# Kernel tuning notes

Measured on AMD Instinct MI355X. Metric: run time of the kernel, lower is better.

## Reference

```python
import jax, jax.numpy as jnp
import numpy as np

TOP_K = 2
NUM_EXPERTS = 64
TEMPERATURE = 1.0

def setup_inputs() -> dict:
    key = jax.random.key(0)
    ks = jax.random.split(key, 4)
    B, L, D, DT, E = 4, 4096, 2048, 16, NUM_EXPERTS
    return {
        "x": jax.random.normal(ks[0], (B, L, D), dtype=jnp.float32),
        "z_task": jax.random.normal(ks[1], (B, DT), dtype=jnp.float32),
        "W_router": jax.random.normal(ks[2], (E, D + DT), dtype=jnp.float32) * 0.02,
        "W_task_proj": jax.random.normal(ks[3], (DT, DT), dtype=jnp.float32) * 0.25,
        "b_task_proj": jnp.zeros((DT,), dtype=jnp.float32),
        "expert_bias": jnp.zeros((E,), dtype=jnp.float32),
    }

def reference(x, z_task, W_router, W_task_proj, b_task_proj, expert_bias):
    B, L, D = x.shape
    E = W_router.shape[0]
    DT = z_task.shape[-1]
    # task_proj: Linear(d_task, d_task) + exact GELU
    tp = jax.nn.gelu(z_task @ W_task_proj.T + b_task_proj, approximate=False)  # [B, DT]
    # concat fusion: logits = [x ; task_proj] @ W_router^T, split to avoid materializing concat
    logits = (jnp.einsum('bld,ed->ble', x, W_router[:, :D])
              + jnp.einsum('bt,et->be', tp, W_router[:, D:])[:, None, :]
              + expert_bias)  # [B, L, E]
    probs = jax.nn.softmax(logits / TEMPERATURE, axis=-1)
    topw, topi = jax.lax.top_k(probs, TOP_K)  # [B, L, K]
    topw = topw / (topw.sum(axis=-1, keepdims=True) + 1e-8)
    # aux load-balance loss: E * sum_i f_i * P_i over flattened tokens
    mask = jax.nn.one_hot(topi, E, dtype=probs.dtype).sum(axis=-2) / TOP_K  # [B, L, E]
    f = mask.reshape(-1, E).mean(axis=0)
    P = probs.reshape(-1, E).mean(axis=0)
    aux_loss = E * (f * P).sum()
    return topw, topi, probs, aux_loss
```

## Files before the change

kernel.cpp:

```cpp
#include <hip/hip_runtime.h>
#include <math.h>


#define DDIM 2048
#define WROW 2064

typedef unsigned int u32;
typedef unsigned short u16;
typedef unsigned long long u64;
using short8 = __attribute__((ext_vector_type(8))) short;
using f32x4  = __attribute__((ext_vector_type(4))) float;

typedef const __attribute__((address_space(1))) u32* gp1;
typedef __attribute__((address_space(3))) u32* lp3;

#define BAR() do {                                                              \
        __builtin_amdgcn_s_barrier();                                           \
        asm volatile("" ::: "memory");                                          \
        __builtin_amdgcn_sched_barrier(0);                                      \
    } while (0)

__device__ __forceinline__ u16 bf16rne(float f) {
    u32 u = __float_as_uint(f);
    return (u16)((u + 0x7FFFu + ((u >> 16) & 1u)) >> 16);
}

__global__ void k0_wsplit(const float* __restrict__ Wr, u32* __restrict__ wh,
                          u32* __restrict__ wl) {
    const int g = blockIdx.x * 256 + threadIdx.x;
    const int e  = g >> 10;
    const int kp = g & 1023;
    const int k  = kp * 2;
    const int step = k >> 5, kb = (k >> 3) & 3, d = (k >> 1) & 3;
    const int grp = e >> 4, lane = kb * 16 + (e & 15);
    const float w0 = Wr[(size_t)e * WROW + k];
    const float w1 = Wr[(size_t)e * WROW + k + 1];
    const u16 h0 = bf16rne(w0);
    const u16 h1 = bf16rne(w1);
    const u16 l0 = bf16rne(w0 - __uint_as_float((u32)h0 << 16));
    const u16 l1 = bf16rne(w1 - __uint_as_float((u32)h1 << 16));
    const u32 oi = (u32)(((step * 4 + grp) * 64 + lane) * 4 + d);
    wh[oi] = ((u32)h1 << 16) | h0;
    wl[oi] = ((u32)l1 << 16) | l0;
}

__global__ void k1_task(const float* __restrict__ z, const float* __restrict__ Wp,
                        const float* __restrict__ bp, const float* __restrict__ Wr,
                        const float* __restrict__ eb, float* __restrict__ wsb) {
    __shared__ float tp[4][16];
    const int t = threadIdx.x;
    if (t < 64) {
        const int b = t >> 4, r = t & 15;
        float s = bp[r];
        #pragma unroll
        for (int i = 0; i < 16; ++i) s += z[b * 16 + i] * Wp[r * 16 + i];
        tp[b][r] = 0.5f * s * (1.0f + erff(s * 0.70710678118654752440f));
    }
    #pragma unroll
    for (int i = t; i < 1024; i += 256) wsb[256 + i] = 0.0f;
    __syncthreads();
    {
        const int b = t >> 6, e = t & 63;
        const float* wr = Wr + (size_t)e * WROW + DDIM;
        float s = eb[e];
        #pragma unroll
        for (int i = 0; i < 16; ++i) s += tp[b][i] * wr[i];
        wsb[b * 64 + e] = s;
    }
}

__global__ __launch_bounds__(576, 1) void k2_mfma(const float* __restrict__ x,
                                                  const float* __restrict__ wsb,
                                                  const u32* __restrict__ whp,
                                                  const u32* __restrict__ wlp,
                                                  float* __restrict__ wacc,
                                                  float* __restrict__ out) {
    __shared__ __align__(16) u32 smem[13312];
    float* const lgf = (float*)smem;
    float* const pff = (float*)&smem[12288];

    const int tid   = threadIdx.x;
    const int wv    = __builtin_amdgcn_readfirstlane(tid >> 6);
    const int lane  = tid & 63;
    const int tok0b = blockIdx.x * 64;
    const int bb    = tok0b >> 12;

    if (wv == 8) {
#define BDMA(t, buf) do {                                                       \
            _Pragma("unroll")                                                   \
            for (int hl = 0; hl < 2; ++hl)                                      \
            _Pragma("unroll")                                                   \
            for (int hh = 0; hh < 2; ++hh)                                      \
            _Pragma("unroll")                                                   \
            for (int g = 0; g < 4; ++g) {                                       \
                const u32* _s = (hl ? wlp : whp) +                              \
                                ((t) + hh * 32) * 1024 + g * 256 + lane * 4;    \
                u32* _d = &smem[(buf) * 4096 + hl * 2048 + hh * 1024 + g * 256 + lane * 4];\
                __builtin_amdgcn_global_load_lds((gp1)_s, (lp3)_d, 16, 0, 0);   \
            }                                                                   \
        } while (0)
        BDMA(0, 0);
        asm volatile("s_waitcnt vmcnt(0)" ::: "memory");
        BAR();
        BDMA(1, 1); BDMA(2, 2);
        for (int t = 0; t < 32; ++t) {
            if (t <= 29)      asm volatile("s_waitcnt vmcnt(16)" ::: "memory");
            else if (t == 30) asm volatile("s_waitcnt vmcnt(0)"  ::: "memory");
            BAR();
            if (t + 3 < 32) BDMA(t + 3, (t + 3) % 3);
        }
#undef BDMA
    } else {
        const int tg  = wv & 3;
        const int h   = wv >> 2;
        const int row = lane & 15;
        const int kg  = lane >> 4;
        const int tok0 = tok0b + tg * 16;

        f32x4 acc[4];
        #pragma unroll
        for (int g = 0; g < 4; ++g) {
            const float tl = (h == 0) ? wsb[bb * 64 + g * 16 + row] : 0.0f;
            acc[g] = (f32x4){tl, tl, tl, tl};
        }
        #pragma unroll
        for (int g = 0; g < 4; ++g) asm volatile("" : "+v"(acc[g]));
        __builtin_amdgcn_sched_barrier(0);

        const u64 xaddr = (u64)(x + (size_t)(tok0 + row) * DDIM + h * 1024 + kg * 8);
        f32x4 xr[6][2];

#define XLOAD(i, T) do {                                                        \
            asm volatile("global_load_dwordx4 %0, %1, off offset:%c2"           \
                : "=&v"(xr[i][0]) : "v"(xaddr), "i"((T) * 128));                \
            asm volatile("global_load_dwordx4 %0, %1, off offset:%c2"           \
                : "=&v"(xr[i][1]) : "v"(xaddr), "i"((T) * 128 + 16));           \
        } while (0)

#define XWAIT(i) do {                                                           \
            asm volatile("s_waitcnt vmcnt(10)"                                  \
                : "+v"(xr[i][0]), "+v"(xr[i][1]));                              \
            __builtin_amdgcn_sched_barrier(0);                                  \
        } while (0)

#define MSTEP(xa, xb, BH, BL) do {                                              \
            float vv[8];                                                        \
            _Pragma("unroll")                                                   \
            for (int j = 0; j < 4; ++j) { vv[j] = (xa)[j]; vv[4 + j] = (xb)[j]; }\
            short8 Ah, Al;                                                      \
            _Pragma("unroll")                                                   \
            for (int j = 0; j < 8; ++j) {                                       \
                const float v = vv[j];                                          \
                const u16 hh = bf16rne(v);                                      \
                const u16 ll = bf16rne(v - __uint_as_float((u32)hh << 16));     \
                Ah[j] = (short)hh; Al[j] = (short)ll;                           \
            }                                                                   \
            _Pragma("unroll")                                                   \
            for (int g = 0; g < 4; ++g) {                                       \
                acc[g] = __builtin_amdgcn_mfma_f32_16x16x32_bf16(Ah, BH[g], acc[g], 0, 0, 0); \
                acc[g] = __builtin_amdgcn_mfma_f32_16x16x32_bf16(Ah, BL[g], acc[g], 0, 0, 0); \
                acc[g] = __builtin_amdgcn_mfma_f32_16x16x32_bf16(Al, BH[g], acc[g], 0, 0, 0); \
                acc[g] = __builtin_amdgcn_mfma_f32_16x16x32_bf16(Al, BL[g], acc[g], 0, 0, 0); \
            }                                                                   \
        } while (0)

        XLOAD(0, 0); XLOAD(1, 1); XLOAD(2, 2);
        XLOAD(3, 3); XLOAD(4, 4); XLOAD(5, 5);
        BAR();
        #pragma unroll
        for (int t = 0; t < 32; ++t) {
            short8 BH[4], BL[4];
            #pragma unroll
            for (int g = 0; g < 4; ++g) {
                BH[g] = *(const short8*)&smem[(t % 3) * 4096 + h * 1024 + g * 256 + lane * 4];
                BL[g] = *(const short8*)&smem[(t % 3) * 4096 + 2048 + h * 1024 + g * 256 + lane * 4];
            }
            XWAIT(t % 6);
            MSTEP(xr[t % 6][0], xr[t % 6][1], BH, BL);
            XLOAD(t % 6, (t + 6) & 31);
            BAR();
        }
        asm volatile("s_waitcnt vmcnt(0)"
            : "+v"(xr[0][0]), "+v"(xr[0][1]), "+v"(xr[1][0]), "+v"(xr[1][1]),
              "+v"(xr[2][0]), "+v"(xr[2][1]), "+v"(xr[3][0]), "+v"(xr[3][1]),
              "+v"(xr[4][0]), "+v"(xr[4][1]), "+v"(xr[5][0]), "+v"(xr[5][1]));
        __builtin_amdgcn_sched_barrier(0);
#undef XLOAD
#undef XWAIT
#undef MSTEP

        #pragma unroll
        for (int g = 0; g < 4; ++g)
            #pragma unroll
            for (int r = 0; r < 4; ++r)
                lgf[h * 4352 + (tg * 16 + kg * 4 + r) * 68 + g * 16 + row] = acc[g][r];
    }

    __syncthreads();

    if (wv < 8) {
        float pacc = 0.0f, facc = 0.0f;
        for (int i = 0; i < 8; ++i) {
            const int tk = wv * 8 + i;
            const float v = lgf[tk * 68 + lane] + lgf[4352 + tk * 68 + lane];
            float m1 = v; int i1 = lane;
            #pragma unroll
            for (int off = 32; off; off >>= 1) {
                const float ov = __shfl_xor(m1, off, 64);
                const int   oi = __shfl_xor(i1, off, 64);
                if (ov > m1 || (ov == m1 && oi < i1)) { m1 = ov; i1 = oi; }
            }
            const float vx = (lane == i1) ? -3.4e38f : v;
            float m2 = vx; int i2 = lane;
            #pragma unroll
            for (int off = 32; off; off >>= 1) {
                const float ov = __shfl_xor(m2, off, 64);
                const int   oi = __shfl_xor(i2, off, 64);
                if (ov > m2 || (ov == m2 && oi < i2)) { m2 = ov; i2 = oi; }
            }
            const float p = __expf(v - m1);
            float s = p;
            #pragma unroll
            for (int off = 32; off; off >>= 1) s += __shfl_xor(s, off, 64);
            const float rZ = 1.0f / s;
            const float pn = p * rZ;
            const int   T  = tok0b + tk;
            out[65536 + (size_t)T * 64 + lane] = pn;
            pacc += pn;
            facc += (lane == i1 ? 1.0f : 0.0f) + (lane == i2 ? 1.0f : 0.0f);
            if (lane == 0) {
                const float q1 = rZ, q2 = __expf(m2 - m1) * rZ;
                const float dn = 1.0f / (q1 + q2 + 1e-8f);
                float2 tw; tw.x = q1 * dn; tw.y = q2 * dn;
                *(float2*)(out + (size_t)T * 2) = tw;
                float2 ti; ti.x = (float)i1; ti.y = (float)i2;
                *(float2*)(out + 32768 + (size_t)T * 2) = ti;
            }
        }
        pff[wv * 128 + lane]      = pacc;
        pff[wv * 128 + 64 + lane] = facc;
    }
    __syncthreads();

    if (wv == 0) {
        float ps = 0.0f, fs = 0.0f;
        #pragma unroll
        for (int w2 = 0; w2 < 8; ++w2) {
            ps += pff[w2 * 128 + lane];
            fs += pff[w2 * 128 + 64 + lane];
        }
        const int slot = blockIdx.x & 7;
        atomicAdd(wacc + slot * 128 + lane, ps);
        atomicAdd(wacc + slot * 128 + 64 + lane, fs);
    }
}

__global__ void k3_aux(const float* __restrict__ wsb, float* __restrict__ out) {
    const int e = threadIdx.x;
    float P = 0.0f, F = 0.0f;
    #pragma unroll
    for (int s = 0; s < 8; ++s) {
        P += wsb[256 + s * 128 + e];
        F += wsb[256 + s * 128 + 64 + e];
    }
    float val = P * F;
    #pragma unroll
    for (int off = 32; off; off >>= 1) val += __shfl_xor(val, off, 64);
    if (e == 0)
        out[1114112] = 64.0f * val / (16384.0f * 2.0f * 16384.0f);
}

extern "C" void kernel_launch(void* const* d_in, const int* in_sizes, int n_in,
                              void* d_out, int out_size, void* d_ws, size_t ws_size,
                              hipStream_t stream) {
    (void)in_sizes; (void)n_in; (void)out_size; (void)ws_size;
    const float* x  = (const float*)d_in[0];
    const float* z  = (const float*)d_in[1];
    const float* Wr = (const float*)d_in[2];
    const float* Wp = (const float*)d_in[3];
    const float* bp = (const float*)d_in[4];
    const float* eb = (const float*)d_in[5];
    float* out = (float*)d_out;
    float* wsb = (float*)d_ws;
    u32*   wfH = (u32*)(wsb + 1280);
    u32*   wfL = wfH + 65536;

    hipLaunchKernelGGL(k0_wsplit, dim3(256), dim3(256), 0, stream, Wr, wfH, wfL);
    hipLaunchKernelGGL(k1_task,   dim3(1),   dim3(256), 0, stream, z, Wp, bp, Wr, eb, wsb);
    hipLaunchKernelGGL(k2_mfma,   dim3(256), dim3(576), 0, stream, x, wsb,
                       wfH, wfL, wsb + 256, out);
    hipLaunchKernelGGL(k3_aux,    dim3(1),   dim3(64),  0, stream, wsb, out);
}
```

Baseline: 49.75 us.

## Merge prep kernels, deepen weight LDS ring, use hardware bf16 packed split

Merges the weight-split and task-projection kernels into one launch with an extra block, which removes one kernel launch. Changes the LDS weight ring from 3 to 4 buffers, so the DMA wave keeps three steps in flight. The x register prefetch goes from 6 to 4 slots using a rolling base pointer. The per-element bf16 hi/lo split now uses v_cvt_pk_bf16_f32 instructions instead of integer rounding. In exchange the kernel uses more LDS and has a shallower x prefetch, and the barrier counts between the DMA wave and the compute waves must stay matched.

```diff
diff --git a/kernel.cpp b/kernel.cpp
--- a/kernel.cpp
+++ b/kernel.cpp
@@ -10,6 +10,7 @@
 typedef unsigned long long u64;
 using short8 = __attribute__((ext_vector_type(8))) short;
 using f32x4  = __attribute__((ext_vector_type(4))) float;
+using u32x4  = __attribute__((ext_vector_type(4))) u32;
 
 typedef const __attribute__((address_space(1))) u32* gp1;
 typedef __attribute__((address_space(3))) u32* lp3;
@@ -25,47 +26,46 @@
     return (u16)((u + 0x7FFFu + ((u >> 16) & 1u)) >> 16);
 }
 
-__global__ void k0_wsplit(const float* __restrict__ Wr, u32* __restrict__ wh,
-                          u32* __restrict__ wl) {
-    const int g = blockIdx.x * 256 + threadIdx.x;
-    const int e  = g >> 10;
-    const int kp = g & 1023;
-    const int k  = kp * 2;
-    const int step = k >> 5, kb = (k >> 3) & 3, d = (k >> 1) & 3;
-    const int grp = e >> 4, lane = kb * 16 + (e & 15);
-    const float w0 = Wr[(size_t)e * WROW + k];
-    const float w1 = Wr[(size_t)e * WROW + k + 1];
-    const u16 h0 = bf16rne(w0);
-    const u16 h1 = bf16rne(w1);
-    const u16 l0 = bf16rne(w0 - __uint_as_float((u32)h0 << 16));
-    const u16 l1 = bf16rne(w1 - __uint_as_float((u32)h1 << 16));
-    const u32 oi = (u32)(((step * 4 + grp) * 64 + lane) * 4 + d);
-    wh[oi] = ((u32)h1 << 16) | h0;
-    wl[oi] = ((u32)l1 << 16) | l0;
-}
-
-__global__ void k1_task(const float* __restrict__ z, const float* __restrict__ Wp,
-                        const float* __restrict__ bp, const float* __restrict__ Wr,
-                        const float* __restrict__ eb, float* __restrict__ wsb) {
-    __shared__ float tp[4][16];
+__global__ void k01_prep(const float* __restrict__ Wr, u32* __restrict__ wh,
+                         u32* __restrict__ wl, const float* __restrict__ z,
+                         const float* __restrict__ Wp, const float* __restrict__ bp,
+                         const float* __restrict__ eb, float* __restrict__ wsb) {
     const int t = threadIdx.x;
-    if (t < 64) {
-        const int b = t >> 4, r = t & 15;
-        float s = bp[r];
-        #pragma unroll
-        for (int i = 0; i < 16; ++i) s += z[b * 16 + i] * Wp[r * 16 + i];
-        tp[b][r] = 0.5f * s * (1.0f + erff(s * 0.70710678118654752440f));
-    }
-    #pragma unroll
-    for (int i = t; i < 1024; i += 256) wsb[256 + i] = 0.0f;
-    __syncthreads();
-    {
-        const int b = t >> 6, e = t & 63;
-        const float* wr = Wr + (size_t)e * WROW + DDIM;
-        float s = eb[e];
-        #pragma unroll
-        for (int i = 0; i < 16; ++i) s += tp[b][i] * wr[i];
-        wsb[b * 64 + e] = s;
+    if (blockIdx.x < 256) {
+        const int g = blockIdx.x * 256 + t;
+        const int e  = g >> 10;
+        const int k  = (g & 1023) * 2;
+        const int step = k >> 5, kb = (k >> 3) & 3, d = (k >> 1) & 3;
+        const int grp = e >> 4, lane = kb * 16 + (e & 15);
+        const float w0 = Wr[(size_t)e * WROW + k];
+        const float w1 = Wr[(size_t)e * WROW + k + 1];
+        const u16 h0 = bf16rne(w0);
+        const u16 h1 = bf16rne(w1);
+        const u16 l0 = bf16rne(w0 - __uint_as_float((u32)h0 << 16));
+        const u16 l1 = bf16rne(w1 - __uint_as_float((u32)h1 << 16));
+        const u32 oi = (u32)(((step * 4 + grp) * 64 + lane) * 4 + d);
+        wh[oi] = ((u32)h1 << 16) | h0;
+        wl[oi] = ((u32)l1 << 16) | l0;
+    } else {
+        __shared__ float tp[4][16];
+        if (t < 64) {
+            const int b = t >> 4, r = t & 15;
+            float s = bp[r];
+            #pragma unroll
+            for (int i = 0; i < 16; ++i) s += z[b * 16 + i] * Wp[r * 16 + i];
+            tp[b][r] = 0.5f * s * (1.0f + erff(s * 0.70710678118654752440f));
+        }
+        #pragma unroll
+        for (int i = t; i < 1024; i += 256) wsb[256 + i] = 0.0f;
+        __syncthreads();
+        {
+            const int b = t >> 6, e = t & 63;
+            const float* wr = Wr + (size_t)e * WROW + DDIM;
+            float s = eb[e];
+            #pragma unroll
+            for (int i = 0; i < 16; ++i) s += tp[b][i] * wr[i];
+            wsb[b * 64 + e] = s;
+        }
     }
 }
 
@@ -75,9 +75,9 @@
                                                   const u32* __restrict__ wlp,
                                                   float* __restrict__ wacc,
                                                   float* __restrict__ out) {
-    __shared__ __align__(16) u32 smem[13312];
+    __shared__ __align__(16) u32 smem[17408];
     float* const lgf = (float*)smem;
-    float* const pff = (float*)&smem[12288];
+    float* const pff = (float*)&smem[16384];
 
     const int tid   = threadIdx.x;
     const int wv    = __builtin_amdgcn_readfirstlane(tid >> 6);
@@ -99,17 +99,26 @@
                 __builtin_amdgcn_global_load_lds((gp1)_s, (lp3)_d, 16, 0, 0);   \
             }                                                                   \
         } while (0)
-        BDMA(0, 0);
-        asm volatile("s_waitcnt vmcnt(0)" ::: "memory");
+#define PSTEP(t, j) do {                                                        \
+            BDMA((t) + 3, ((j) + 3) & 3);                                       \
+            asm volatile("s_waitcnt vmcnt(32)" ::: "memory");                   \
+            BAR();                                                              \
+        } while (0)
+        BDMA(0, 0); BDMA(1, 1); BDMA(2, 2);
+        asm volatile("s_waitcnt vmcnt(32)" ::: "memory");
         BAR();
-        BDMA(1, 1); BDMA(2, 2);
-        for (int t = 0; t < 32; ++t) {
-            if (t <= 29)      asm volatile("s_waitcnt vmcnt(16)" ::: "memory");
-            else if (t == 30) asm volatile("s_waitcnt vmcnt(0)"  ::: "memory");
-            BAR();
-            if (t + 3 < 32) BDMA(t + 3, (t + 3) % 3);
-        }
+        for (int g7 = 0; g7 < 7; ++g7) {
+            const int t0 = g7 * 4;
+            PSTEP(t0 + 0, 0); PSTEP(t0 + 1, 1);
+            PSTEP(t0 + 2, 2); PSTEP(t0 + 3, 3);
+        }
+        BDMA(31, 3);
+        asm volatile("s_waitcnt vmcnt(32)" ::: "memory"); BAR();
+        asm volatile("s_waitcnt vmcnt(16)" ::: "memory"); BAR();
+        asm volatile("s_waitcnt vmcnt(0)"  ::: "memory"); BAR();
+        BAR();
 #undef BDMA
+#undef PSTEP
     } else {
         const int tg  = wv & 3;
         const int h   = wv >> 2;
@@ -127,34 +136,36 @@
         for (int g = 0; g < 4; ++g) asm volatile("" : "+v"(acc[g]));
         __builtin_amdgcn_sched_barrier(0);
 
-        const u64 xaddr = (u64)(x + (size_t)(tok0 + row) * DDIM + h * 1024 + kg * 8);
-        f32x4 xr[6][2];
-
-#define XLOAD(i, T) do {                                                        \
-            asm volatile("global_load_dwordx4 %0, %1, off offset:%c2"           \
-                : "=&v"(xr[i][0]) : "v"(xaddr), "i"((T) * 128));                \
-            asm volatile("global_load_dwordx4 %0, %1, off offset:%c2"           \
-                : "=&v"(xr[i][1]) : "v"(xaddr), "i"((T) * 128 + 16));           \
-        } while (0)
-
-#define XWAIT(i) do {                                                           \
-            asm volatile("s_waitcnt vmcnt(10)"                                  \
-                : "+v"(xr[i][0]), "+v"(xr[i][1]));                              \
-            __builtin_amdgcn_sched_barrier(0);                                  \
+        u64 xcur = (u64)(x + (size_t)(tok0 + row) * DDIM + h * 1024 + kg * 8);
+        f32x4 xr[4][2];
+
+#define SPLIT(xa, xb, Ah, Al) do {                                              \
+            u32 h0_, h1_, h2_, h3_, l0_, l1_, l2_, l3_;                         \
+            asm("v_cvt_pk_bf16_f32 %0, %1, %2" : "=v"(h0_) : "v"((xa)[0]), "v"((xa)[1])); \
+            asm("v_cvt_pk_bf16_f32 %0, %1, %2" : "=v"(h1_) : "v"((xa)[2]), "v"((xa)[3])); \
+            asm("v_cvt_pk_bf16_f32 %0, %1, %2" : "=v"(h2_) : "v"((xb)[0]), "v"((xb)[1])); \
+            asm("v_cvt_pk_bf16_f32 %0, %1, %2" : "=v"(h3_) : "v"((xb)[2]), "v"((xb)[3])); \
+            const float r0_ = (xa)[0] - __uint_as_float(h0_ << 16);             \
+            const float r1_ = (xa)[1] - __uint_as_float(h0_ & 0xFFFF0000u);     \
+            const float r2_ = (xa)[2] - __uint_as_float(h1_ << 16);             \
+            const float r3_ = (xa)[3] - __uint_as_float(h1_ & 0xFFFF0000u);     \
+            const float r4_ = (xb)[0] - __uint_as_float(h2_ << 16);             \
+            const float r5_ = (xb)[1] - __uint_as_float(h2_ & 0xFFFF0000u);     \
+            const float r6_ = (xb)[2] - __uint_as_float(h3_ << 16);             \
+            const float r7_ = (xb)[3] - __uint_as_float(h3_ & 0xFFFF0000u);     \
+            asm("v_cvt_pk_bf16_f32 %0, %1, %2" : "=v"(l0_) : "v"(r0_), "v"(r1_)); \
+            asm("v_cvt_pk_bf16_f32 %0, %1, %2" : "=v"(l1_) : "v"(r2_), "v"(r3_)); \
+            asm("v_cvt_pk_bf16_f32 %0, %1, %2" : "=v"(l2_) : "v"(r4_), "v"(r5_)); \
+            asm("v_cvt_pk_bf16_f32 %0, %1, %2" : "=v"(l3_) : "v"(r6_), "v"(r7_)); \
+            const u32x4 uh_ = {h0_, h1_, h2_, h3_};                             \
+            const u32x4 ul_ = {l0_, l1_, l2_, l3_};                             \
+            Ah = __builtin_bit_cast(short8, uh_);                               \
+            Al = __builtin_bit_cast(short8, ul_);                               \
         } while (0)
 
 #define MSTEP(xa, xb, BH, BL) do {                                              \
-            float vv[8];                                                        \
-            _Pragma("unroll")                                                   \
-            for (int j = 0; j < 4; ++j) { vv[j] = (xa)[j]; vv[4 + j] = (xb)[j]; }\
             short8 Ah, Al;                                                      \
-            _Pragma("unroll")                                                   \
-            for (int j = 0; j < 8; ++j) {                                       \
-                const float v = vv[j];                                          \
-                const u16 hh = bf16rne(v);                                      \
-                const u16 ll = bf16rne(v - __uint_as_float((u32)hh << 16));     \
-                Ah[j] = (short)hh; Al[j] = (short)ll;                           \
-            }                                                                   \
+            SPLIT(xa, xb, Ah, Al);                                              \
             _Pragma("unroll")                                                   \
             for (int g = 0; g < 4; ++g) {                                       \
                 acc[g] = __builtin_amdgcn_mfma_f32_16x16x32_bf16(Ah, BH[g], acc[g], 0, 0, 0); \
@@ -164,30 +175,42 @@
             }                                                                   \
         } while (0)
 
-        XLOAD(0, 0); XLOAD(1, 1); XLOAD(2, 2);
-        XLOAD(3, 3); XLOAD(4, 4); XLOAD(5, 5);
+#define CSTEP(j, WAITN, DOLOAD) do {                                            \
+            short8 BH[4], BL[4];                                                \
+            _Pragma("unroll")                                                   \
+            for (int g2 = 0; g2 < 4; ++g2) {                                    \
+                BH[g2] = *(const short8*)&smem[(j) * 4096 + h * 1024 + g2 * 256 + lane * 4]; \
+                BL[g2] = *(const short8*)&smem[(j) * 4096 + 2048 + h * 1024 + g2 * 256 + lane * 4]; \
+            }                                                                   \
+            asm volatile("s_waitcnt vmcnt(" #WAITN ")"                          \
+                : "+v"(xr[j][0]), "+v"(xr[j][1]));                              \
+            __builtin_amdgcn_sched_barrier(0);                                  \
+            MSTEP(xr[j][0], xr[j][1], BH, BL);                                  \
+            if (DOLOAD) {                                                       \
+                asm volatile("global_load_dwordx4 %0, %1, off offset:%c2"       \
+                    : "=&v"(xr[j][0]) : "v"(xcur), "i"(((j) + 4) * 128));       \
+                asm volatile("global_load_dwordx4 %0, %1, off offset:%c2"       \
+                    : "=&v"(xr[j][1]) : "v"(xcur), "i"(((j) + 4) * 128 + 16));  \
+            }                                                                   \
+            BAR();                                                              \
+        } while (0)
+
+        #pragma unroll
+        for (int j = 0; j < 4; ++j) {
+            asm volatile("global_load_dwordx4 %0, %1, off offset:%c2"
+                : "=&v"(xr[j][0]) : "v"(xcur), "i"(j * 128));
+            asm volatile("global_load_dwordx4 %0, %1, off offset:%c2"
+                : "=&v"(xr[j][1]) : "v"(xcur), "i"(j * 128 + 16));
+        }
         BAR();
-        #pragma unroll
-        for (int t = 0; t < 32; ++t) {
-            short8 BH[4], BL[4];
-            #pragma unroll
-            for (int g = 0; g < 4; ++g) {
-                BH[g] = *(const short8*)&smem[(t % 3) * 4096 + h * 1024 + g * 256 + lane * 4];
-                BL[g] = *(const short8*)&smem[(t % 3) * 4096 + 2048 + h * 1024 + g * 256 + lane * 4];
-            }
-            XWAIT(t % 6);
-            MSTEP(xr[t % 6][0], xr[t % 6][1], BH, BL);
-            XLOAD(t % 6, (t + 6) & 31);
-            BAR();
-        }
-        asm volatile("s_waitcnt vmcnt(0)"
-            : "+v"(xr[0][0]), "+v"(xr[0][1]), "+v"(xr[1][0]), "+v"(xr[1][1]),
-              "+v"(xr[2][0]), "+v"(xr[2][1]), "+v"(xr[3][0]), "+v"(xr[3][1]),
-              "+v"(xr[4][0]), "+v"(xr[4][1]), "+v"(xr[5][0]), "+v"(xr[5][1]));
-        __builtin_amdgcn_sched_barrier(0);
-#undef XLOAD
-#undef XWAIT
+        for (int g7 = 0; g7 < 7; ++g7) {
+            CSTEP(0, 6, 1); CSTEP(1, 6, 1); CSTEP(2, 6, 1); CSTEP(3, 6, 1);
+            xcur += 512;
+        }
+        CSTEP(0, 6, 0); CSTEP(1, 4, 0); CSTEP(2, 2, 0); CSTEP(3, 0, 0);
+#undef SPLIT
 #undef MSTEP
+#undef CSTEP
 
         #pragma unroll
         for (int g = 0; g < 4; ++g)
@@ -285,9 +308,9 @@
     u32*   wfH = (u32*)(wsb + 1280);
     u32*   wfL = wfH + 65536;
 
-    hipLaunchKernelGGL(k0_wsplit, dim3(256), dim3(256), 0, stream, Wr, wfH, wfL);
-    hipLaunchKernelGGL(k1_task,   dim3(1),   dim3(256), 0, stream, z, Wp, bp, Wr, eb, wsb);
-    hipLaunchKernelGGL(k2_mfma,   dim3(256), dim3(576), 0, stream, x, wsb,
+    hipLaunchKernelGGL(k01_prep, dim3(257), dim3(256), 0, stream,
+                       Wr, wfH, wfL, z, Wp, bp, eb, wsb);
+    hipLaunchKernelGGL(k2_mfma,  dim3(256), dim3(576), 0, stream, x, wsb,
                        wfH, wfL, wsb + 256, out);
-    hipLaunchKernelGGL(k3_aux,    dim3(1),   dim3(64),  0, stream, wsb, out);
-}
+    hipLaunchKernelGGL(k3_aux,   dim3(1),   dim3(64),  0, stream, wsb, out);
+}
```

After: 46.04 us, median of 2. 7.5% less time.
